# Performance work log

Measured on AMD Instinct MI355X. Metric: run time of the kernel, lower is better.

Reference implementation:

```python
import jax, jax.numpy as jnp
import numpy as np

VOCAB = 30000
K1 = 1.2
B_PARAM = 0.75


def setup_inputs() -> dict:
    key = jax.random.key(0)
    k1, k2 = jax.random.split(key)
    B, L = 2048, 512
    input_ids = jax.random.randint(k1, (B, L), 0, VOCAB, dtype=jnp.int64)
    attention_mask = jnp.ones((B, L), dtype=jnp.int64)
    W = jax.random.normal(k2, (768, VOCAB), dtype=jnp.float32) / np.sqrt(VOCAB)
    return {"input_ids": input_ids, "attention_mask": attention_mask, "W": W}


def reference(input_ids, attention_mask, W):
    B, L = input_ids.shape
    # valid tokens: attended AND 100 < id < VOCAB
    valid = (attention_mask == 1) & (input_ids > 100) & (input_ids < VOCAB)
    validf = valid.astype(jnp.float32)
    doc_len = validf.sum(-1)  # [B]

    # batched histogram (TF counts) via scatter-add; invalid entries add 0 at slot 0
    rows = jnp.broadcast_to(jnp.arange(B)[:, None], (B, L))
    toks = jnp.where(valid, input_ids, 0)
    tf = jnp.zeros((B, VOCAB), jnp.float32).at[rows, toks].add(validf)  # [B, VOCAB]

    # BM25 scoring; torch writes scores only at unique tokens -> equivalent to masking tf>0
    length_norm = jnp.maximum(1.0 + B_PARAM * (doc_len / 100.0 - 1.0), 0.5)[:, None]
    scores = jnp.where(tf > 0, tf * (K1 + 1.0) / (tf + K1 * length_norm), 0.0)

    v = scores + 1e-10
    v = v / jnp.linalg.norm(v, axis=-1, keepdims=True)  # F.normalize p=2

    out = v @ W.T  # Linear(VOCAB, 768, bias=False)
    out = out / jnp.linalg.norm(out, axis=-1, keepdims=True)
    return out
```

## Files before the change

kernel.cpp:

```cpp
#include <hip/hip_runtime.h>
#include <hip/hip_bf16.h>
#include <stdint.h>

#define B_ROWS 2048
#define SEQ 512
#define VOC 30000
#define DMODEL 768
#define K1 1.2f
#define BPAR 0.75f
#define NT 192
#define PF 8

__launch_bounds__(256)
__global__ void transpose_W256(const float* __restrict__ W, __hip_bfloat16* __restrict__ Wb) {
    __shared__ __hip_bfloat16 tile[64][258];
    int tBase = blockIdx.x * 256;
    int jBase = blockIdx.y * 64;
    int tx = threadIdx.x;
    int ty = threadIdx.y;

#pragma unroll
    for (int jj = 0; jj < 16; jj++) {
        int j = jBase + jj * 4 + ty;
        int t = tBase + tx * 4;
        if (t < VOC) {
            float4 v = *(const float4*)(W + (size_t)j * VOC + t);
            int c = tx * 4;
            tile[jj * 4 + ty][c]     = __float2bfloat16(v.x);
            tile[jj * 4 + ty][c + 1] = __float2bfloat16(v.y);
            tile[jj * 4 + ty][c + 2] = __float2bfloat16(v.z);
            tile[jj * 4 + ty][c + 3] = __float2bfloat16(v.w);
        }
    }
    __syncthreads();

#pragma unroll
    for (int i = 0; i < 64; i++) {
        int trow = i * 4 + ty;
        int t = tBase + trow;
        if (t < VOC) {
            Wb[(size_t)t * DMODEL + jBase + tx] = tile[tx][trow];
        }
    }
}

__device__ __forceinline__ float b2f(unsigned short h) {
    union { uint32_t u; float f; } v; v.u = ((uint32_t)h) << 16; return v.f;
}

__launch_bounds__(NT, 6)
__global__ void bm25_main(const int* __restrict__ ids, const int* __restrict__ mask,
                          const __hip_bfloat16* __restrict__ Wb,
                          float* __restrict__ out) {
    __shared__ int   stoks[SEQ];
    __shared__ float wts[SEQ];
    __shared__ int   nv;
    __shared__ float wred[3];

    int b = blockIdx.x;
    int tid = threadIdx.x;

    if (tid == 0) nv = 0;
    __syncthreads();

    for (int i = tid; i < SEQ; i += NT) {
        int id = ids[(size_t)b * SEQ + i];
        int m  = mask[(size_t)b * SEQ + i];
        if (m == 1 && id > 100 && id < VOC) {
            stoks[atomicAdd(&nv, 1)] = id;
        }
    }
    __syncthreads();
    int n = nv;

    for (int i = n + tid; i < SEQ; i += NT) stoks[i] = 0x7fffffff;

    for (int k = 2; k <= SEQ; k <<= 1) {
        for (int j = k >> 1; j > 0; j >>= 1) {
            __syncthreads();
            for (int i = tid; i < SEQ; i += NT) {
                int ixj = i ^ j;
                if (ixj > i) {
                    int a = stoks[i], c = stoks[ixj];
                    if ((a > c) == ((i & k) == 0)) { stoks[i] = c; stoks[ixj] = a; }
                }
            }
        }
    }
    __syncthreads();

    float kln = K1 * fmaxf(1.0f + BPAR * ((float)n / 100.0f - 1.0f), 0.5f);
    for (int i = tid; i < n; i += NT) {
        int t = stoks[i];
        int lo = i; while (lo > 0 && stoks[lo - 1] == t) lo--;
        int hi = i; while (hi < n - 1 && stoks[hi + 1] == t) hi++;
        wts[i] = (K1 + 1.0f) / ((float)(hi - lo + 1) + kln);
    }
    __syncthreads();

    const ushort4* __restrict__ Wb4 = (const ushort4*)Wb;
    float4 acc = make_float4(0.f, 0.f, 0.f, 0.f);
    int p = 0;
    for (; p + PF <= n; p += PF) {
        ushort4 r[PF];
        float   w[PF];
#pragma unroll
        for (int q = 0; q < PF; q++) {
            r[q] = Wb4[(size_t)stoks[p + q] * (DMODEL / 4) + tid];
            w[q] = wts[p + q];
        }
#pragma unroll
        for (int q = 0; q < PF; q++) {
            acc.x = fmaf(w[q], b2f(r[q].x), acc.x);
            acc.y = fmaf(w[q], b2f(r[q].y), acc.y);
            acc.z = fmaf(w[q], b2f(r[q].z), acc.z);
            acc.w = fmaf(w[q], b2f(r[q].w), acc.w);
        }
    }
    for (; p < n; p++) {
        float w = wts[p];
        ushort4 r = Wb4[(size_t)stoks[p] * (DMODEL / 4) + tid];
        acc.x = fmaf(w, b2f(r.x), acc.x);
        acc.y = fmaf(w, b2f(r.y), acc.y);
        acc.z = fmaf(w, b2f(r.z), acc.z);
        acc.w = fmaf(w, b2f(r.w), acc.w);
    }

    float ss = acc.x * acc.x + acc.y * acc.y + acc.z * acc.z + acc.w * acc.w;
#pragma unroll
    for (int off = 32; off > 0; off >>= 1) ss += __shfl_down(ss, off);
    if ((tid & 63) == 0) wred[tid >> 6] = ss;
    __syncthreads();
    float inv = rsqrtf(fmaxf(wred[0] + wred[1] + wred[2], 1e-30f));

    float4 o;
    o.x = acc.x * inv; o.y = acc.y * inv; o.z = acc.z * inv; o.w = acc.w * inv;
    ((float4*)(out + (size_t)b * DMODEL))[tid] = o;
}

extern "C" void kernel_launch(void* const* d_in, const int* in_sizes, int n_in,
                              void* d_out, int out_size, void* d_ws, size_t ws_size,
                              hipStream_t stream) {
    const int*   ids  = (const int*)d_in[0];
    const int*   mask = (const int*)d_in[1];
    const float* W    = (const float*)d_in[2];
    float* out = (float*)d_out;

    __hip_bfloat16* Wb = (__hip_bfloat16*)d_ws;

    dim3 tgrid((VOC + 255) / 256, DMODEL / 64);
    dim3 tblock(64, 4);
    transpose_W256<<<tgrid, tblock, 0, stream>>>(W, Wb);

    bm25_main<<<B_ROWS, NT, 0, stream>>>(ids, mask, Wb, out);
}
```

Measured before the change: 152.9 us.

## Split per-row gather-accumulate across two blocks and combine partials

Each row's sparse gather over bf16 W rows is split into two blocks that take alternating tokens, so twice as many blocks are in flight. Each block writes a partial 768-vector to workspace, and a new combine kernel sums the two halves and applies the L2 normalisation. The price is that both halves repeat the token filtering, bitonic sort and weight computation, plus an extra launch and a round trip of the partials through global memory.

```diff
diff --git a/kernel.cpp b/kernel.cpp
--- a/kernel.cpp
+++ b/kernel.cpp
@@ -49,15 +49,17 @@
 }
 
 __launch_bounds__(NT, 6)
-__global__ void bm25_main(const int* __restrict__ ids, const int* __restrict__ mask,
+__global__ void bm25_half(const int* __restrict__ ids, const int* __restrict__ mask,
                           const __hip_bfloat16* __restrict__ Wb,
-                          float* __restrict__ out) {
+                          float* __restrict__ part) {
     __shared__ int   stoks[SEQ];
     __shared__ float wts[SEQ];
+    __shared__ int   hstoks[SEQ / 2];
+    __shared__ float hwts[SEQ / 2];
     __shared__ int   nv;
-    __shared__ float wred[3];
 
-    int b = blockIdx.x;
+    int b    = blockIdx.x & (B_ROWS - 1);
+    int half = blockIdx.x >> 11;
     int tid = threadIdx.x;
 
     if (tid == 0) nv = 0;
@@ -98,16 +100,24 @@
     }
     __syncthreads();
 
+    int m = (n + 1 - half) >> 1;
+    for (int i = tid; i < m; i += NT) {
+        int p = (i << 1) | half;
+        hstoks[i] = stoks[p];
+        hwts[i]   = wts[p];
+    }
+    __syncthreads();
+
     const ushort4* __restrict__ Wb4 = (const ushort4*)Wb;
     float4 acc = make_float4(0.f, 0.f, 0.f, 0.f);
     int p = 0;
-    for (; p + PF <= n; p += PF) {
+    for (; p + PF <= m; p += PF) {
         ushort4 r[PF];
         float   w[PF];
 #pragma unroll
         for (int q = 0; q < PF; q++) {
-            r[q] = Wb4[(size_t)stoks[p + q] * (DMODEL / 4) + tid];
-            w[q] = wts[p + q];
+            r[q] = Wb4[(size_t)hstoks[p + q] * (DMODEL / 4) + tid];
+            w[q] = hwts[p + q];
         }
 #pragma unroll
         for (int q = 0; q < PF; q++) {
@@ -117,14 +127,28 @@
             acc.w = fmaf(w[q], b2f(r[q].w), acc.w);
         }
     }
-    for (; p < n; p++) {
-        float w = wts[p];
-        ushort4 r = Wb4[(size_t)stoks[p] * (DMODEL / 4) + tid];
+    for (; p < m; p++) {
+        float w = hwts[p];
+        ushort4 r = Wb4[(size_t)hstoks[p] * (DMODEL / 4) + tid];
         acc.x = fmaf(w, b2f(r.x), acc.x);
         acc.y = fmaf(w, b2f(r.y), acc.y);
         acc.z = fmaf(w, b2f(r.z), acc.z);
         acc.w = fmaf(w, b2f(r.w), acc.w);
     }
+
+    ((float4*)(part + ((size_t)half * B_ROWS + b) * DMODEL))[tid] = acc;
+}
+
+__launch_bounds__(NT)
+__global__ void bm25_combine(const float* __restrict__ part, float* __restrict__ out) {
+    __shared__ float wred[3];
+    int b = blockIdx.x;
+    int tid = threadIdx.x;
+
+    float4 a0 = ((const float4*)(part + (size_t)b * DMODEL))[tid];
+    float4 a1 = ((const float4*)(part + ((size_t)B_ROWS + b) * DMODEL))[tid];
+    float4 acc;
+    acc.x = a0.x + a1.x; acc.y = a0.y + a1.y; acc.z = a0.z + a1.z; acc.w = a0.w + a1.w;
 
     float ss = acc.x * acc.x + acc.y * acc.y + acc.z * acc.z + acc.w * acc.w;
 #pragma unroll
@@ -147,10 +171,13 @@
     float* out = (float*)d_out;
 
     __hip_bfloat16* Wb = (__hip_bfloat16*)d_ws;
+    float* part = (float*)((char*)d_ws + (size_t)VOC * DMODEL * sizeof(__hip_bfloat16));
 
     dim3 tgrid((VOC + 255) / 256, DMODEL / 64);
     dim3 tblock(64, 4);
     transpose_W256<<<tgrid, tblock, 0, stream>>>(W, Wb);
 
-    bm25_main<<<B_ROWS, NT, 0, stream>>>(ids, mask, Wb, out);
+    bm25_half<<<B_ROWS * 2, NT, 0, stream>>>(ids, mask, Wb, part);
+
+    bm25_combine<<<B_ROWS, NT, 0, stream>>>(part, out);
 }
```

Result: slower. 224.4 us (+46.7%).

## Move per-row sort and BM25 weighting into transpose kernel launch

Applied to the files above, without the earlier changes.

Merges the W transpose/bf16 conversion and the per-row token filtering, bitonic sort and BM25 weight computation into one launch that uses disjoint block ranges. The row preprocessing can then overlap with the bandwidth-bound transpose instead of running serially before the gather. The gather kernel only reads the precomputed sorted row offsets and weights from workspace. This adds a global-memory round trip for tokens and weights and a larger combined launch in exchange.

```diff
diff --git a/kernel.cpp b/kernel.cpp
--- a/kernel.cpp
+++ b/kernel.cpp
@@ -10,37 +10,99 @@
 #define BPAR 0.75f
 #define NT 192
 #define PF 8
+#define TGX 118
+#define TGY 12
+#define TTILES (TGX * TGY)
 
 __launch_bounds__(256)
-__global__ void transpose_W256(const float* __restrict__ W, __hip_bfloat16* __restrict__ Wb) {
-    __shared__ __hip_bfloat16 tile[64][258];
-    int tBase = blockIdx.x * 256;
-    int jBase = blockIdx.y * 64;
-    int tx = threadIdx.x;
-    int ty = threadIdx.y;
+__global__ void prep_all(const float* __restrict__ W, __hip_bfloat16* __restrict__ Wb,
+                         const int* __restrict__ ids, const int* __restrict__ mask,
+                         int* __restrict__ stoks_g, float* __restrict__ wts_g,
+                         int* __restrict__ n_g) {
+    __shared__ ushort smem[64 * 258];
+    int bid = blockIdx.x;
+    int tid = threadIdx.x;
+
+    if (bid < TTILES) {
+        ushort (*tile)[258] = (ushort(*)[258])smem;
+        int bx = bid % TGX, by = bid / TGX;
+        int tBase = bx * 256;
+        int jBase = by * 64;
+        int tx = tid & 63;
+        int ty = tid >> 6;
 
 #pragma unroll
-    for (int jj = 0; jj < 16; jj++) {
-        int j = jBase + jj * 4 + ty;
-        int t = tBase + tx * 4;
-        if (t < VOC) {
-            float4 v = *(const float4*)(W + (size_t)j * VOC + t);
-            int c = tx * 4;
-            tile[jj * 4 + ty][c]     = __float2bfloat16(v.x);
-            tile[jj * 4 + ty][c + 1] = __float2bfloat16(v.y);
-            tile[jj * 4 + ty][c + 2] = __float2bfloat16(v.z);
-            tile[jj * 4 + ty][c + 3] = __float2bfloat16(v.w);
+        for (int jj = 0; jj < 16; jj++) {
+            int j = jBase + jj * 4 + ty;
+            int t = tBase + tx * 4;
+            if (t < VOC) {
+                float4 v = *(const float4*)(W + (size_t)j * VOC + t);
+                int c = tx * 4;
+                tile[jj * 4 + ty][c]     = __bfloat16_as_ushort(__float2bfloat16(v.x));
+                tile[jj * 4 + ty][c + 1] = __bfloat16_as_ushort(__float2bfloat16(v.y));
+                tile[jj * 4 + ty][c + 2] = __bfloat16_as_ushort(__float2bfloat16(v.z));
+                tile[jj * 4 + ty][c + 3] = __bfloat16_as_ushort(__float2bfloat16(v.w));
+            }
         }
-    }
-    __syncthreads();
+        __syncthreads();
 
 #pragma unroll
-    for (int i = 0; i < 64; i++) {
-        int trow = i * 4 + ty;
-        int t = tBase + trow;
-        if (t < VOC) {
-            Wb[(size_t)t * DMODEL + jBase + tx] = tile[tx][trow];
+        for (int i = 0; i < 64; i++) {
+            int trow = i * 4 + ty;
+            int t = tBase + trow;
+            if (t < VOC) {
+                ((ushort*)Wb)[(size_t)t * DMODEL + jBase + tx] = tile[tx][trow];
+            }
         }
+    } else {
+        int b = bid - TTILES;
+        int*   stoks = (int*)smem;
+        float* wts   = (float*)((char*)smem + 2048);
+        int*   nvp   = (int*)((char*)smem + 4096);
+
+        if (tid == 0) *nvp = 0;
+        __syncthreads();
+
+        for (int i = tid; i < SEQ; i += 256) {
+            int id = ids[(size_t)b * SEQ + i];
+            int m  = mask[(size_t)b * SEQ + i];
+            if (m == 1 && id > 100 && id < VOC) {
+                stoks[atomicAdd(nvp, 1)] = id;
+            }
+        }
+        __syncthreads();
+        int n = *nvp;
+
+        for (int i = n + tid; i < SEQ; i += 256) stoks[i] = 0x7fffffff;
+
+        for (int k = 2; k <= SEQ; k <<= 1) {
+            for (int j = k >> 1; j > 0; j >>= 1) {
+                __syncthreads();
+                for (int i = tid; i < SEQ; i += 256) {
+                    int ixj = i ^ j;
+                    if (ixj > i) {
+                        int a = stoks[i], c = stoks[ixj];
+                        if ((a > c) == ((i & k) == 0)) { stoks[i] = c; stoks[ixj] = a; }
+                    }
+                }
+            }
+        }
+        __syncthreads();
+
+        float kln = K1 * fmaxf(1.0f + BPAR * ((float)n / 100.0f - 1.0f), 0.5f);
+        for (int i = tid; i < n; i += 256) {
+            int t = stoks[i];
+            int lo = i; while (lo > 0 && stoks[lo - 1] == t) lo--;
+            int hi = i; while (hi < n - 1 && stoks[hi + 1] == t) hi++;
+            wts[i] = (K1 + 1.0f) / ((float)(hi - lo + 1) + kln);
+        }
+        __syncthreads();
+
+        for (int i = tid; i < n; i += 256) {
+            stoks_g[(size_t)b * SEQ + i] = stoks[i] * (DMODEL / 4);
+            wts_g[(size_t)b * SEQ + i]   = wts[i];
+        }
+        if (tid == 0) n_g[b] = n;
     }
 }
 
@@ -49,52 +111,21 @@
 }
 
 __launch_bounds__(NT, 6)
-__global__ void bm25_main(const int* __restrict__ ids, const int* __restrict__ mask,
-                          const __hip_bfloat16* __restrict__ Wb,
-                          float* __restrict__ out) {
+__global__ void bm25_gather(const int* __restrict__ stoks_g, const float* __restrict__ wts_g,
+                            const int* __restrict__ n_g,
+                            const __hip_bfloat16* __restrict__ Wb,
+                            float* __restrict__ out) {
     __shared__ int   stoks[SEQ];
     __shared__ float wts[SEQ];
-    __shared__ int   nv;
     __shared__ float wred[3];
 
     int b = blockIdx.x;
     int tid = threadIdx.x;
+    int n = n_g[b];
 
-    if (tid == 0) nv = 0;
-    __syncthreads();
-
-    for (int i = tid; i < SEQ; i += NT) {
-        int id = ids[(size_t)b * SEQ + i];
-        int m  = mask[(size_t)b * SEQ + i];
-        if (m == 1 && id > 100 && id < VOC) {
-            stoks[atomicAdd(&nv, 1)] = id;
-        }
-    }
-    __syncthreads();
-    int n = nv;
-
-    for (int i = n + tid; i < SEQ; i += NT) stoks[i] = 0x7fffffff;
-
-    for (int k = 2; k <= SEQ; k <<= 1) {
-        for (int j = k >> 1; j > 0; j >>= 1) {
-            __syncthreads();
-            for (int i = tid; i < SEQ; i += NT) {
-                int ixj = i ^ j;
-                if (ixj > i) {
-                    int a = stoks[i], c = stoks[ixj];
-                    if ((a > c) == ((i & k) == 0)) { stoks[i] = c; stoks[ixj] = a; }
-                }
-            }
-        }
-    }
-    __syncthreads();
-
-    float kln = K1 * fmaxf(1.0f + BPAR * ((float)n / 100.0f - 1.0f), 0.5f);
     for (int i = tid; i < n; i += NT) {
-        int t = stoks[i];
-        int lo = i; while (lo > 0 && stoks[lo - 1] == t) lo--;
-        int hi = i; while (hi < n - 1 && stoks[hi + 1] == t) hi++;
-        wts[i] = (K1 + 1.0f) / ((float)(hi - lo + 1) + kln);
+        stoks[i] = stoks_g[(size_t)b * SEQ + i];
+        wts[i]   = wts_g[(size_t)b * SEQ + i];
     }
     __syncthreads();
 
@@ -106,7 +137,7 @@
         float   w[PF];
 #pragma unroll
         for (int q = 0; q < PF; q++) {
-            r[q] = Wb4[(size_t)stoks[p + q] * (DMODEL / 4) + tid];
+            r[q] = Wb4[(size_t)stoks[p + q] + tid];
             w[q] = wts[p + q];
         }
 #pragma unroll
@@ -119,7 +150,7 @@
     }
     for (; p < n; p++) {
         float w = wts[p];
-        ushort4 r = Wb4[(size_t)stoks[p] * (DMODEL / 4) + tid];
+        ushort4 r = Wb4[(size_t)stoks[p] + tid];
         acc.x = fmaf(w, b2f(r.x), acc.x);
         acc.y = fmaf(w, b2f(r.y), acc.y);
         acc.z = fmaf(w, b2f(r.z), acc.z);
@@ -146,11 +177,14 @@
     const float* W    = (const float*)d_in[2];
     float* out = (float*)d_out;
 
-    __hip_bfloat16* Wb = (__hip_bfloat16*)d_ws;
+    char* ws = (char*)d_ws;
+    __hip_bfloat16* Wb = (__hip_bfloat16*)ws;
+    size_t off = (size_t)VOC * DMODEL * sizeof(__hip_bfloat16);
+    int*   stoks_g = (int*)(ws + off);        off += (size_t)B_ROWS * SEQ * 4;
+    float* wts_g   = (float*)(ws + off);      off += (size_t)B_ROWS * SEQ * 4;
+    int*   n_g     = (int*)(ws + off);
 
-    dim3 tgrid((VOC + 255) / 256, DMODEL / 64);
-    dim3 tblock(64, 4);
-    transpose_W256<<<tgrid, tblock, 0, stream>>>(W, Wb);
+    prep_all<<<TTILES + B_ROWS, 256, 0, stream>>>(W, Wb, ids, mask, stoks_g, wts_g, n_g);
 
-    bm25_main<<<B_ROWS, NT, 0, stream>>>(ids, mask, Wb, out);
+    bm25_gather<<<B_ROWS, NT, 0, stream>>>(stoks_g, wts_g, n_g, Wb, out);
 }
```

Measured after the change: 160.3 us. 4.8% more time.

## Split per-document sort and weight computation into a separate prep kernel

Applied to the files above, without the earlier changes.

Moves token filtering, the bitonic sort and the BM25 weight computation out of the gather kernel into a separate 256-thread kernel. That kernel writes pre-scaled row offsets, weights and counts to workspace, so the gather kernel only loads them and does the weighted row sums. The aim is to shorten the gather kernel and run the sort with a wider block. The cost is an extra launch plus a global-memory round trip for the intermediate arrays.

```diff
diff --git a/kernel.cpp b/kernel.cpp
--- a/kernel.cpp
+++ b/kernel.cpp
@@ -10,6 +10,62 @@
 #define BPAR 0.75f
 #define NT 192
 #define PF 8
+
+__launch_bounds__(256)
+__global__ void prep_docs(const int* __restrict__ ids, const int* __restrict__ mask,
+                          int* __restrict__ stoks_g, float* __restrict__ wts_g,
+                          int* __restrict__ n_g) {
+    __shared__ int   stoks[SEQ];
+    __shared__ float wts[SEQ];
+    __shared__ int   nv;
+
+    int b = blockIdx.x;
+    int tid = threadIdx.x;
+
+    if (tid == 0) nv = 0;
+    __syncthreads();
+
+    for (int i = tid; i < SEQ; i += 256) {
+        int id = ids[(size_t)b * SEQ + i];
+        int m  = mask[(size_t)b * SEQ + i];
+        if (m == 1 && id > 100 && id < VOC) {
+            stoks[atomicAdd(&nv, 1)] = id;
+        }
+    }
+    __syncthreads();
+    int n = nv;
+
+    for (int i = n + tid; i < SEQ; i += 256) stoks[i] = 0x7fffffff;
+
+    for (int k = 2; k <= SEQ; k <<= 1) {
+        for (int j = k >> 1; j > 0; j >>= 1) {
+            __syncthreads();
+            for (int i = tid; i < SEQ; i += 256) {
+                int ixj = i ^ j;
+                if (ixj > i) {
+                    int a = stoks[i], c = stoks[ixj];
+                    if ((a > c) == ((i & k) == 0)) { stoks[i] = c; stoks[ixj] = a; }
+                }
+            }
+        }
+    }
+    __syncthreads();
+
+    float kln = K1 * fmaxf(1.0f + BPAR * ((float)n / 100.0f - 1.0f), 0.5f);
+    for (int i = tid; i < n; i += 256) {
+        int t = stoks[i];
+        int lo = i; while (lo > 0 && stoks[lo - 1] == t) lo--;
+        int hi = i; while (hi < n - 1 && stoks[hi + 1] == t) hi++;
+        wts[i] = (K1 + 1.0f) / ((float)(hi - lo + 1) + kln);
+    }
+    __syncthreads();
+
+    for (int i = tid; i < n; i += 256) {
+        stoks_g[(size_t)b * SEQ + i] = stoks[i] * (DMODEL / 4);
+        wts_g[(size_t)b * SEQ + i]   = wts[i];
+    }
+    if (tid == 0) n_g[b] = n;
+}
 
 __launch_bounds__(256)
 __global__ void transpose_W256(const float* __restrict__ W, __hip_bfloat16* __restrict__ Wb) {
@@ -49,52 +105,21 @@
 }
 
 __launch_bounds__(NT, 6)
-__global__ void bm25_main(const int* __restrict__ ids, const int* __restrict__ mask,
-                          const __hip_bfloat16* __restrict__ Wb,
-                          float* __restrict__ out) {
+__global__ void bm25_gather(const int* __restrict__ stoks_g, const float* __restrict__ wts_g,
+                            const int* __restrict__ n_g,
+                            const __hip_bfloat16* __restrict__ Wb,
+                            float* __restrict__ out) {
     __shared__ int   stoks[SEQ];
     __shared__ float wts[SEQ];
-    __shared__ int   nv;
     __shared__ float wred[3];
 
     int b = blockIdx.x;
     int tid = threadIdx.x;
+    int n = n_g[b];
 
-    if (tid == 0) nv = 0;
-    __syncthreads();
-
-    for (int i = tid; i < SEQ; i += NT) {
-        int id = ids[(size_t)b * SEQ + i];
-        int m  = mask[(size_t)b * SEQ + i];
-        if (m == 1 && id > 100 && id < VOC) {
-            stoks[atomicAdd(&nv, 1)] = id;
-        }
-    }
-    __syncthreads();
-    int n = nv;
-
-    for (int i = n + tid; i < SEQ; i += NT) stoks[i] = 0x7fffffff;
-
-    for (int k = 2; k <= SEQ; k <<= 1) {
-        for (int j = k >> 1; j > 0; j >>= 1) {
-            __syncthreads();
-            for (int i = tid; i < SEQ; i += NT) {
-                int ixj = i ^ j;
-                if (ixj > i) {
-                    int a = stoks[i], c = stoks[ixj];
-                    if ((a > c) == ((i & k) == 0)) { stoks[i] = c; stoks[ixj] = a; }
-                }
-            }
-        }
-    }
-    __syncthreads();
-
-    float kln = K1 * fmaxf(1.0f + BPAR * ((float)n / 100.0f - 1.0f), 0.5f);
     for (int i = tid; i < n; i += NT) {
-        int t = stoks[i];
-        int lo = i; while (lo > 0 && stoks[lo - 1] == t) lo--;
-        int hi = i; while (hi < n - 1 && stoks[hi + 1] == t) hi++;
-        wts[i] = (K1 + 1.0f) / ((float)(hi - lo + 1) + kln);
+        stoks[i] = stoks_g[(size_t)b * SEQ + i];
+        wts[i]   = wts_g[(size_t)b * SEQ + i];
     }
     __syncthreads();
 
@@ -106,7 +131,7 @@
         float   w[PF];
 #pragma unroll
         for (int q = 0; q < PF; q++) {
-            r[q] = Wb4[(size_t)stoks[p + q] * (DMODEL / 4) + tid];
+            r[q] = Wb4[(size_t)stoks[p + q] + tid];
             w[q] = wts[p + q];
         }
 #pragma unroll
@@ -119,7 +144,7 @@
     }
     for (; p < n; p++) {
         float w = wts[p];
-        ushort4 r = Wb4[(size_t)stoks[p] * (DMODEL / 4) + tid];
+        ushort4 r = Wb4[(size_t)stoks[p] + tid];
         acc.x = fmaf(w, b2f(r.x), acc.x);
         acc.y = fmaf(w, b2f(r.y), acc.y);
         acc.z = fmaf(w, b2f(r.z), acc.z);
@@ -146,11 +171,18 @@
     const float* W    = (const float*)d_in[2];
     float* out = (float*)d_out;
 
-    __hip_bfloat16* Wb = (__hip_bfloat16*)d_ws;
+    char* ws = (char*)d_ws;
+    __hip_bfloat16* Wb = (__hip_bfloat16*)ws;
+    size_t off = (size_t)VOC * DMODEL * sizeof(__hip_bfloat16);
+    int*   stoks_g = (int*)(ws + off);        off += (size_t)B_ROWS * SEQ * 4;
+    float* wts_g   = (float*)(ws + off);      off += (size_t)B_ROWS * SEQ * 4;
+    int*   n_g     = (int*)(ws + off);
+
+    prep_docs<<<B_ROWS, 256, 0, stream>>>(ids, mask, stoks_g, wts_g, n_g);
 
     dim3 tgrid((VOC + 255) / 256, DMODEL / 64);
     dim3 tblock(64, 4);
     transpose_W256<<<tgrid, tblock, 0, stream>>>(W, Wb);
 
-    bm25_main<<<B_ROWS, NT, 0, stream>>>(ids, mask, Wb, out);
+    bm25_gather<<<B_ROWS, NT, 0, stream>>>(stoks_g, wts_g, n_g, Wb, out);
 }
```

New measurement: 152.6 us. About the same (-0.2%).
